# Kernel tuning notes

Hardware: AMD Instinct MI355X
Metric: run time of the kernel (lower is better)

## Reference

```python
import jax, jax.numpy as jnp
import numpy as np
from jax import lax

VOCAB = 32000
N_E = 1024
N_D = 1024
DEPTH = 4
L = 512
B = 8
HIGHWAY_BIAS = -3.0  # args.bias, folded into forget-gate bias


def setup_inputs() -> dict:
    key = jax.random.key(0)
    ks = jax.random.split(key, 8)
    x = jax.random.randint(ks[0], (L, B), 0, VOCAB)
    hidden = jnp.zeros((DEPTH, B, N_D), dtype=jnp.float32)
    emb = jax.random.normal(ks[1], (VOCAB, N_E), dtype=jnp.float32) * (3.0 / VOCAB) ** 0.5
    W0 = jax.random.normal(ks[2], (N_E, 4 * N_D), dtype=jnp.float32) * N_E ** -0.5
    Wl = jax.random.normal(ks[3], (DEPTH - 1, N_D, 3 * N_D), dtype=jnp.float32) * N_D ** -0.5
    vc = jax.random.normal(ks[4], (DEPTH, 2 * N_D), dtype=jnp.float32) * 0.1
    out_W = jax.random.normal(ks[5], (N_D, VOCAB), dtype=jnp.float32) * (3.0 / VOCAB) ** 0.5
    out_b = jnp.zeros((VOCAB,), dtype=jnp.float32)
    return {"x": x, "hidden": hidden, "emb": emb, "W0": W0, "Wl": Wl,
            "vc": vc, "out_W": out_W, "out_b": out_b}


def _sru_layer(u0, u1, u2, resid, vf, vr, c0):
    # u*: (L, B, d) precomputed GEMM outputs; scan only does elementwise recurrence.
    def step(c, inp):
        u0t, u1t, u2t, rt = inp
        f = jax.nn.sigmoid(u1t + vf * c + HIGHWAY_BIAS)
        r = jax.nn.sigmoid(u2t + vr * c)
        c_new = f * c + (1.0 - f) * u0t
        h = r * c_new + (1.0 - r) * rt
        return c_new, h
    c_last, hs = lax.scan(step, c0, (u0, u1, u2, resid))
    return hs, c_last


def reference(x, hidden, emb, W0, Wl, vc, out_W, out_b):
    h = emb[x]  # (L, B, n_e); dropout disabled (p=0)
    c_finals = []
    for layer in range(DEPTH):
        if layer == 0:
            U = jnp.einsum('lbe,ek->lbk', h, W0).reshape(L, B, 4, N_D)
            resid = U[:, :, 3]  # k=4: transformed input as highway residual
        else:
            U = jnp.einsum('lbd,dk->lbk', h, Wl[layer - 1]).reshape(L, B, 3, N_D)
            resid = h           # k=3: highway residual is the layer input
        vf = vc[layer, :N_D]
        vr = vc[layer, N_D:]
        h, c_last = _sru_layer(U[:, :, 0], U[:, :, 1], U[:, :, 2], resid, vf, vr, hidden[layer])
        c_finals.append(c_last)
    out = h.reshape(L * B, N_D) @ out_W + out_b  # (L*B, vocab)
    return out, jnp.stack(c_finals)
```

## Files before the change

kernel.cpp:

```cpp
#include <hip/hip_runtime.h>
#include <hip/hip_bf16.h>

#define L_SEQ 512
#define BATCH 8
#define ND 1024
#define VOCAB_N 32000
#define MROWS 4096
#define KDIM 1024
#define BK 64
#define NKT (KDIM / BK)
#define NKS 32
#define NSCAN 128

typedef unsigned short u16;
typedef unsigned int u32;
using bf16x8 = __attribute__((ext_vector_type(8))) __bf16;
using f32x4  = __attribute__((ext_vector_type(4))) float;
using u16x8  = __attribute__((ext_vector_type(8))) unsigned short;
using u16x4  = __attribute__((ext_vector_type(4))) unsigned short;

#define BAR() asm volatile("s_barrier" ::: "memory")
#define VMW(n) asm volatile("s_waitcnt vmcnt(" #n ")" ::: "memory")
#define SCHED() __builtin_amdgcn_sched_barrier(0)

static __device__ __forceinline__ u16 f2bf(float f) {
  u32 u = __builtin_bit_cast(u32, f);
  u32 r = u + 0x7FFF + ((u >> 16) & 1);
  return (u16)(r >> 16);
}
static __device__ __forceinline__ float bf2f(u16 b) {
  u32 u = ((u32)b) << 16;
  return __builtin_bit_cast(float, u);
}
static __device__ __forceinline__ void gload16(const void* g, void* l) {
  __builtin_amdgcn_global_load_lds(
      (const __attribute__((address_space(1))) void*)g,
      (__attribute__((address_space(3))) void*)l, 16, 0, 0);
}

static __device__ __forceinline__ void transpose_body(int tb, const float* __restrict__ W,
                                                      u16* __restrict__ Wt, int Ndim) {
  __shared__ float s[32][33];
  int nx = Ndim >> 5;
  int n0 = (tb % nx) * 32, k0 = (tb / nx) * 32;
  int tid = threadIdx.x;
  int tx = tid & 31, ty = tid >> 5;
#pragma unroll
  for (int i = 0; i < 4; i++)
    s[ty * 4 + i][tx] = __builtin_nontemporal_load(
        &W[(size_t)(k0 + ty * 4 + i) * Ndim + n0 + tx]);
  __syncthreads();
  int n = tid >> 3, kg = tid & 7;
  u16x4 o;
#pragma unroll
  for (int j = 0; j < 4; j++) o[j] = f2bf(s[kg * 4 + j][n]);
  *(u16x4*)(Wt + (size_t)(n0 + n) * KDIM + k0 + kg * 4) = o;
}

__global__ __launch_bounds__(256) void k_embed_t(const int* __restrict__ x,
                                                 const float* __restrict__ emb,
                                                 u16* __restrict__ h,
                                                 const float* __restrict__ Wsrc,
                                                 u16* __restrict__ WtOut, int NdimT) {
  if (blockIdx.x >= 2048) {
    transpose_body(blockIdx.x - 2048, Wsrc, WtOut, NdimT);
    return;
  }
  int t = blockIdx.x * 256 + threadIdx.x;
  int fidx = t * 8;
  int row = fidx >> 10;
  int col = fidx & 1023;
  int tok = x[row];
  const float4* src = (const float4*)(emb + (size_t)tok * ND + col);
  float4 a = src[0], b = src[1];
  u16x8 o;
  o[0]=f2bf(a.x); o[1]=f2bf(a.y); o[2]=f2bf(a.z); o[3]=f2bf(a.w);
  o[4]=f2bf(b.x); o[5]=f2bf(b.y); o[6]=f2bf(b.z); o[7]=f2bf(b.w);
  *(u16x8*)(h + fidx) = o;
}

__global__ __launch_bounds__(256) void k_transpose_cast(const float* __restrict__ W,
                                                        u16* __restrict__ Wt, int Ndim) {
  transpose_body(blockIdx.x, W, Wt, Ndim);
}

static __device__ __forceinline__ void stage8k(const u16* __restrict__ gbase,
                                               char* sm, int qdst, int tid) {
#pragma unroll
  for (int j = 0; j < 2; ++j) {
    int d = (j * 256 + tid) * 16;
    int o = d ^ (((d >> 7) & 7) << 4);
    gload16(gbase + (size_t)(o >> 7) * KDIM + ((o & 127) >> 1), sm + qdst + d);
  }
}

static __device__ __forceinline__ bf16x8 frag_ld(const char* sm, int base, int r, int cb) {
  int p = (r * 128 + cb) ^ ((r & 7) << 4);
  return *(const bf16x8*)(sm + base + p);
}

static __device__ __forceinline__ bf16x8 frag32(const char* smbase, int r, int cb) {
  int p = r * 64 + cb;
  p ^= ((p >> 7) & 3) << 4;
  return *(const bf16x8*)(smbase + p);
}

__global__ __launch_bounds__(512, 4) void k_gemm_out(const u16* __restrict__ A,
                                                     const u16* __restrict__ Bt,
                                                     float* __restrict__ CoutF, int Ndim,
                                                     const float* __restrict__ bias) {
  extern __shared__ __align__(16) char sm[];

  int bid = blockIdx.x;
  int xcd = bid & 7;
  int i = bid >> 3;
  int bm = (xcd << 2) | (i & 3);
  int bn = i >> 2;
  int m0 = bm * 128, n0 = bn * 256;

  int tid = threadIdx.x;
  int lane = tid & 63, w = tid >> 6;
  int wm = w >> 2, wn = w & 3;
  int l15 = lane & 15, hi16 = lane >> 4;

  f32x4 acc[4][4] = {};
  bf16x8 aA[4], bB[4];

  const u16* Ab = A + (size_t)m0 * KDIM;
  const u16* Bb = Bt + (size_t)n0 * KDIM;

  auto stage = [&](int t, int base) {
    {
      int d = tid * 16;
      int o = d ^ (((d >> 7) & 3) << 4);
      gload16(Ab + (size_t)(o >> 6) * KDIM + t * 32 + ((o & 63) >> 1), sm + base + d);
    }
#pragma unroll
    for (int j = 0; j < 2; ++j) {
      int d = (j * 512 + tid) * 16;
      int o = d ^ (((d >> 7) & 3) << 4);
      gload16(Bb + (size_t)(o >> 6) * KDIM + t * 32 + ((o & 63) >> 1),
              sm + base + 8192 + d);
    }
  };

  stage(0, 0);
  stage(1, 24576);
  VMW(3);
  BAR();

  const int cb = hi16 * 16;
  const int ra = wm * 64 + l15;
  const int rbv = wn * 64 + l15;

  int rb = 0, sb = 2;
#pragma unroll 1
  for (int t = 0; t < NKS; ++t) {
    const bool st = (t + 2 < NKS);
    if (st) stage(t + 2, sb * 24576);
    const char* cur = sm + rb * 24576;
#pragma unroll
    for (int mi = 0; mi < 4; ++mi) aA[mi] = frag32(cur, ra + mi * 16, cb);
#pragma unroll
    for (int ni = 0; ni < 4; ++ni) bB[ni] = frag32(cur + 8192, rbv + ni * 16, cb);
    __builtin_amdgcn_s_setprio(1);
#pragma unroll
    for (int mi = 0; mi < 4; ++mi)
#pragma unroll
      for (int ni = 0; ni < 4; ++ni)
        acc[mi][ni] = __builtin_amdgcn_mfma_f32_16x16x32_bf16(aA[mi], bB[ni], acc[mi][ni], 0, 0, 0);
    __builtin_amdgcn_s_setprio(0);
    SCHED();
    if (st) { VMW(3); } else { VMW(0); }
    BAR();
    rb = (rb == 2) ? 0 : rb + 1;
    sb = (sb == 2) ? 0 : sb + 1;
  }

  float* epi = (float*)sm;
  for (int p = 0; p < 4; ++p) {
    if (p) __syncthreads();
    if (wn == p) {
#pragma unroll
      for (int mi = 0; mi < 4; ++mi)
#pragma unroll
        for (int ni = 0; ni < 4; ++ni)
#pragma unroll
          for (int r = 0; r < 4; ++r)
            epi[(wm * 64 + mi * 16 + hi16 * 4 + r) * 68 + ni * 16 + l15] = acc[mi][ni][r];
    }
    __syncthreads();
    int gcolbase = n0 + p * 64;
#pragma unroll
    for (int i2 = 0; i2 < 4; ++i2) {
      int fidx = i2 * 2048 + tid * 4;
      int row = fidx >> 6, col = fidx & 63;
      f32x4 v = *(const f32x4*)(epi + row * 68 + col);
      int gcol = gcolbase + col;
      const float4 bb = *(const float4*)(bias + gcol);
      v[0] += bb.x; v[1] += bb.y; v[2] += bb.z; v[3] += bb.w;
      __builtin_nontemporal_store(v, (f32x4*)(CoutF + (size_t)(m0 + row) * Ndim + gcol));
    }
  }
}

template <int EPI>
__global__ __launch_bounds__(256, 2) void k_gemm128(const u16* __restrict__ A,
                                                    const u16* __restrict__ Bt,
                                                    u16* __restrict__ Cout, int Ndim) {
  extern __shared__ __align__(16) char sm[];

  int cpx = gridDim.x >> 3;
  int bid = blockIdx.x;
  int wg = (bid & 7) * cpx + (bid >> 3);
  int bm = wg & 31;
  int bn = wg >> 5;
  int m0 = bm * 128, n0 = bn * 128;

  int tid = threadIdx.x;
  int lane = tid & 63, w = tid >> 6;
  int wm = w >> 1, wn = w & 1;
  int l15 = lane & 15, hi16 = lane >> 4;
  const int rA = wm * 64 + l15, rB = wn * 64 + l15;

  f32x4 acc[4][4] = {};
  bf16x8 aA[4][2], bB[4][2];

  const u16* Ab = A + (size_t)m0 * KDIM;
  const u16* Bb = Bt + (size_t)n0 * KDIM;

  auto stage_tile = [&](int t, int buf) {
    int base = buf * 32768;
    stage8k(Ab + t * 64,                     sm, base,         tid);
    stage8k(Ab + (size_t)64 * KDIM + t * 64, sm, base + 8192,  tid);
    stage8k(Bb + t * 64,                     sm, base + 16384, tid);
    stage8k(Bb + (size_t)64 * KDIM + t * 64, sm, base + 24576, tid);
  };

  stage_tile(0, 0);
  VMW(0);
  BAR();

#pragma unroll 1
  for (int t = 0; t < NKT; ++t) {
    int cur = (t & 1) * 32768;
    if (t + 1 < NKT) stage_tile(t + 1, (t & 1) ^ 1);
#pragma unroll
    for (int kk = 0; kk < 2; ++kk) {
      int cb = kk * 64 + hi16 * 16;
#pragma unroll
      for (int mi = 0; mi < 4; ++mi) aA[mi][kk] = frag_ld(sm, cur, rA + mi * 16, cb);
#pragma unroll
      for (int ni = 0; ni < 4; ++ni) bB[ni][kk] = frag_ld(sm, cur + 16384, rB + ni * 16, cb);
    }
    __builtin_amdgcn_s_setprio(1);
#pragma unroll
    for (int kk = 0; kk < 2; ++kk)
#pragma unroll
      for (int mi = 0; mi < 4; ++mi)
#pragma unroll
        for (int ni = 0; ni < 4; ++ni)
          acc[mi][ni] = __builtin_amdgcn_mfma_f32_16x16x32_bf16(aA[mi][kk], bB[ni][kk], acc[mi][ni], 0, 0, 0);
    __builtin_amdgcn_s_setprio(0);
    SCHED();
    VMW(0);
    BAR();
  }

  float* epi = (float*)sm;
  for (int p = 0; p < 2; ++p) {
    if (p) __syncthreads();
    if (wn == p) {
#pragma unroll
      for (int mi = 0; mi < 4; ++mi)
#pragma unroll
        for (int ni = 0; ni < 4; ++ni)
#pragma unroll
          for (int r = 0; r < 4; ++r)
            epi[(wm * 64 + mi * 16 + hi16 * 4 + r) * 68 + ni * 16 + l15] = acc[mi][ni][r];
    }
    __syncthreads();
    int gcolbase = n0 + p * 64;
    int plane = gcolbase >> 10;
#pragma unroll
    for (int i = 0; i < 8; ++i) {
      int fidx = i * 1024 + tid * 4;
      int row = fidx >> 6, col = fidx & 63;
      f32x4 v = *(const f32x4*)(epi + row * 68 + col);
      int gcol = gcolbase + col;
      if (plane == 1) {
#pragma unroll
        for (int j = 0; j < 4; j++) v[j] = -1.44269504f * (v[j] - 3.0f);
      } else if (plane == 2) {
#pragma unroll
        for (int j = 0; j < 4; j++) v[j] = -1.44269504f * v[j];
      }
      u16x4 o;
#pragma unroll
      for (int j = 0; j < 4; j++) o[j] = f2bf(v[j]);
      *(u16x4*)(Cout + (size_t)(m0 + row) * Ndim + gcol) = o;
    }
  }
}

__global__ __launch_bounds__(256) void k_scan(const u16* __restrict__ U, int P,
                                              const u16* __restrict__ resid, int rstride,
                                              u16* __restrict__ hout,
                                              const float* __restrict__ vc,
                                              const float* __restrict__ hidden,
                                              float* __restrict__ cfin, int layer,
                                              const float* __restrict__ Wsrc,
                                              u16* __restrict__ WtOut, int NdimT) {
  if (blockIdx.x >= NSCAN) {
    transpose_body(blockIdx.x - NSCAN, Wsrc, WtOut, NdimT);
    return;
  }
  if (threadIdx.x >= 64) return;
  int cid = blockIdx.x * 64 + threadIdx.x;
  int b = cid >> 10, d = cid & 1023;
  float vfp = -1.44269504f * vc[layer * 2048 + d];
  float vrp = -1.44269504f * vc[layer * 2048 + 1024 + d];
  float c = hidden[layer * 8192 + cid];
  const u16* pu = U + (size_t)b * P * 1024 + d;
  const u16* pr = resid + (size_t)b * rstride + d;
  u16* ph = hout + (size_t)b * 1024 + d;
  const int ustep = P * 1024;
  const int rstep = rstride;

  u16 su0[16], sa1[16], sa2[16], srs[16];
#pragma unroll
  for (int j = 0; j < 16; j++) {
    su0[j] = pu[(size_t)(8 * j) * ustep];
    sa1[j] = pu[(size_t)(8 * j) * ustep + 1024];
    sa2[j] = pu[(size_t)(8 * j) * ustep + 2048];
    srs[j] = pr[(size_t)(8 * j) * rstep];
  }
  for (int tb = 0; tb < L_SEQ; tb += 16) {
#pragma unroll
    for (int j = 0; j < 16; j++) {
      int t = tb + j;
      float u0f = bf2f(su0[j]), a1f = bf2f(sa1[j]);
      float a2f = bf2f(sa2[j]), rf = bf2f(srs[j]);
      int tp = (t + 16) & 511;
      su0[j] = pu[(size_t)(8 * tp) * ustep];
      sa1[j] = pu[(size_t)(8 * tp) * ustep + 1024];
      sa2[j] = pu[(size_t)(8 * tp) * ustep + 2048];
      srs[j] = pr[(size_t)(8 * tp) * rstep];
      float e1 = __builtin_amdgcn_exp2f(fmaf(vfp, c, a1f));
      float e2 = __builtin_amdgcn_exp2f(fmaf(vrp, c, a2f));
      float fv = __builtin_amdgcn_rcpf(1.0f + e1);
      float rv = __builtin_amdgcn_rcpf(1.0f + e2);
      float cn = fmaf(fv, c - u0f, u0f);
      float hv = fmaf(rv, cn - rf, rf);
      ph[(size_t)t * (BATCH * ND)] = f2bf(hv);
      c = cn;
    }
  }
  cfin[layer * 8192 + cid] = c;
}

extern "C" void kernel_launch(void* const* d_in, const int* in_sizes, int n_in,
                              void* d_out, int out_size, void* d_ws, size_t ws_size,
                              hipStream_t stream) {
  const int*   x      = (const int*)d_in[0];
  const float* hidden = (const float*)d_in[1];
  const float* emb    = (const float*)d_in[2];
  const float* W0     = (const float*)d_in[3];
  const float* Wl     = (const float*)d_in[4];
  const float* vc     = (const float*)d_in[5];
  const float* outW   = (const float*)d_in[6];
  const float* outb   = (const float*)d_in[7];
  float* out = (float*)d_out;

  char* ws = (char*)d_ws;
  u16* hA    = (u16*)ws;
  u16* hB    = (u16*)(ws + 8388608);
  u16* U     = (u16*)(ws + 16777216);
  u16* Wt    = (u16*)(ws + 50331648);
  float* cfin = out + (size_t)MROWS * VOCAB_N;

  const size_t wtbig_off_big = 58720256;
  bool bigws = ws_size >= (size_t)(wtbig_off_big + (size_t)VOCAB_N * KDIM * 2);
  u16* WtBig = (u16*)(ws + (bigws ? wtbig_off_big : 16777216));

  k_embed_t<<<2048 + 4096, 256, 0, stream>>>(x, emb, hA, W0, Wt, 4096);

  k_gemm128<0><<<32 * 32, 256, 65536, stream>>>(hA, Wt, U, 4096);
  k_scan<<<NSCAN + 3072, 256, 0, stream>>>(U, 4, U + 3 * 1024, 4 * 1024, hB, vc, hidden,
                                           cfin, 0, Wl, Wt, 3072);

  const u16* hin[3]  = {hB, hA, hB};
  u16*       hout[3] = {hA, hB, hA};
  for (int l = 1; l <= 3; l++) {
    k_gemm128<1><<<32 * 24, 256, 65536, stream>>>(hin[l - 1], Wt, U, 3072);
    if (l < 3) {
      k_scan<<<NSCAN + 3072, 256, 0, stream>>>(U, 3, hin[l - 1], 1024, hout[l - 1], vc,
                                               hidden, cfin, l,
                                               Wl + (size_t)l * KDIM * 3072, Wt, 3072);
    } else if (bigws) {
      k_scan<<<NSCAN + 32000, 256, 0, stream>>>(U, 3, hin[l - 1], 1024, hout[l - 1], vc,
                                                hidden, cfin, l, outW, WtBig, VOCAB_N);
    } else {
      k_scan<<<NSCAN, 256, 0, stream>>>(U, 3, hin[l - 1], 1024, hout[l - 1], vc,
                                        hidden, cfin, l, nullptr, nullptr, 32);
      k_transpose_cast<<<32000, 256, 0, stream>>>(outW, WtBig, VOCAB_N);
    }
  }

  k_gemm_out<<<32 * 125, 512, 73728, stream>>>(hA, WtBig, out, VOCAB_N, outb);
}
```

Measured before the change: 665.1 us.

## Load A fragments directly from global in output GEMM, stage only B in LDS

In the output-projection GEMM kernel, the A tile is no longer staged through shared memory; each wave reads its A fragments straight from global memory into registers. The freed LDS goes to a 4-slot B buffer with prefetch depth 3 instead of 3 slots of A+B, and the B fragment loads are split into two halves to cut register pressure. The aim is to reduce LDS traffic and deepen the pipeline, at the cost of direct global loads for A that may stall MFMA issue and are duplicated across the waves that share the same rows.

Result: slower. 946.0 us (+42.2%).

```diff
diff --git a/kernel.cpp b/kernel.cpp
--- a/kernel.cpp
+++ b/kernel.cpp
@@ -124,59 +124,58 @@
   int l15 = lane & 15, hi16 = lane >> 4;
 
   f32x4 acc[4][4] = {};
-  bf16x8 aA[4], bB[4];
-
-  const u16* Ab = A + (size_t)m0 * KDIM;
+  bf16x8 aA[4], bB[2];
+
   const u16* Bb = Bt + (size_t)n0 * KDIM;
-
-  auto stage = [&](int t, int base) {
-    {
-      int d = tid * 16;
-      int o = d ^ (((d >> 7) & 3) << 4);
-      gload16(Ab + (size_t)(o >> 6) * KDIM + t * 32 + ((o & 63) >> 1), sm + base + d);
-    }
+  const u16* Ap = A + (size_t)(m0 + wm * 64 + l15) * KDIM + hi16 * 8;
+
+  auto stageB = [&](int t, int base) {
 #pragma unroll
     for (int j = 0; j < 2; ++j) {
       int d = (j * 512 + tid) * 16;
       int o = d ^ (((d >> 7) & 3) << 4);
       gload16(Bb + (size_t)(o >> 6) * KDIM + t * 32 + ((o & 63) >> 1),
-              sm + base + 8192 + d);
+              sm + base + d);
     }
   };
 
-  stage(0, 0);
-  stage(1, 24576);
-  VMW(3);
+  stageB(0, 0);
+  stageB(1, 16384);
+  stageB(2, 32768);
+  VMW(4);
   BAR();
 
   const int cb = hi16 * 16;
-  const int ra = wm * 64 + l15;
   const int rbv = wn * 64 + l15;
 
-  int rb = 0, sb = 2;
 #pragma unroll 1
   for (int t = 0; t < NKS; ++t) {
-    const bool st = (t + 2 < NKS);
-    if (st) stage(t + 2, sb * 24576);
-    const char* cur = sm + rb * 24576;
-#pragma unroll
-    for (int mi = 0; mi < 4; ++mi) aA[mi] = frag32(cur, ra + mi * 16, cb);
-#pragma unroll
-    for (int ni = 0; ni < 4; ++ni) bB[ni] = frag32(cur + 8192, rbv + ni * 16, cb);
+    const bool st = (t + 3 < NKS);
+#pragma unroll
+    for (int mi = 0; mi < 4; ++mi)
+      aA[mi] = *(const bf16x8*)(Ap + (size_t)mi * 16 * KDIM + t * 32);
+    if (st) stageB(t + 3, ((t + 3) & 3) * 16384);
+    const char* cur = sm + (t & 3) * 16384;
+
     __builtin_amdgcn_s_setprio(1);
 #pragma unroll
-    for (int mi = 0; mi < 4; ++mi)
-#pragma unroll
-      for (int ni = 0; ni < 4; ++ni)
-        acc[mi][ni] = __builtin_amdgcn_mfma_f32_16x16x32_bf16(aA[mi], bB[ni], acc[mi][ni], 0, 0, 0);
+    for (int h = 0; h < 2; ++h) {
+#pragma unroll
+      for (int j = 0; j < 2; ++j) bB[j] = frag32(cur, rbv + (h * 2 + j) * 16, cb);
+#pragma unroll
+      for (int mi = 0; mi < 4; ++mi)
+#pragma unroll
+        for (int j = 0; j < 2; ++j)
+          acc[mi][h * 2 + j] = __builtin_amdgcn_mfma_f32_16x16x32_bf16(
+              aA[mi], bB[j], acc[mi][h * 2 + j], 0, 0, 0);
+    }
     __builtin_amdgcn_s_setprio(0);
     SCHED();
-    if (st) { VMW(3); } else { VMW(0); }
+    if (st) { VMW(4); } else { VMW(0); }
     BAR();
-    rb = (rb == 2) ? 0 : rb + 1;
-    sb = (sb == 2) ? 0 : sb + 1;
-  }
-
+  }
+
+  __syncthreads();
   float* epi = (float*)sm;
   for (int p = 0; p < 4; ++p) {
     if (p) __syncthreads();
@@ -407,5 +406,5 @@
     }
   }
 
-  k_gemm_out<<<32 * 125, 512, 73728, stream>>>(hA, WtBig, out, VOCAB_N, outb);
-}
+  k_gemm_out<<<32 * 125, 512, 65536, stream>>>(hA, WtBig, out, VOCAB_N, outb);
+}
```

## Switch layer GEMM to triple-buffered BK=32 pipeline with XCD-aware tile mapping

Applied to the files above, without the earlier changes.

The 128x128 layer GEMM now stages K-tiles of 32 instead of 64 and keeps three shared-memory buffers, prefetching two tiles ahead and waiting only on the older loads (vmcnt 4) rather than draining all loads every iteration. Shared memory per block falls from 64KB to 48KB, and the launch bound rises to 3 blocks per CU so occupancy can increase. The block-to-tile mapping is changed so each XCD handles a contiguous group of M tiles, which should improve L2 reuse of the A operand. In exchange there are twice as many barriers per K-loop, and fewer registers are available per thread.

Result: no change. 657.2 us (-1.2%).

```diff
diff --git a/kernel.cpp b/kernel.cpp
--- a/kernel.cpp
+++ b/kernel.cpp
@@ -7,8 +7,6 @@
 #define VOCAB_N 32000
 #define MROWS 4096
 #define KDIM 1024
-#define BK 64
-#define NKT (KDIM / BK)
 #define NKS 32
 #define NSCAN 128
 
@@ -84,21 +82,6 @@
   transpose_body(blockIdx.x, W, Wt, Ndim);
 }
 
-static __device__ __forceinline__ void stage8k(const u16* __restrict__ gbase,
-                                               char* sm, int qdst, int tid) {
-#pragma unroll
-  for (int j = 0; j < 2; ++j) {
-    int d = (j * 256 + tid) * 16;
-    int o = d ^ (((d >> 7) & 7) << 4);
-    gload16(gbase + (size_t)(o >> 7) * KDIM + ((o & 127) >> 1), sm + qdst + d);
-  }
-}
-
-static __device__ __forceinline__ bf16x8 frag_ld(const char* sm, int base, int r, int cb) {
-  int p = (r * 128 + cb) ^ ((r & 7) << 4);
-  return *(const bf16x8*)(sm + base + p);
-}
-
 static __device__ __forceinline__ bf16x8 frag32(const char* smbase, int r, int cb) {
   int p = r * 64 + cb;
   p ^= ((p >> 7) & 3) << 4;
@@ -205,66 +188,76 @@
 }
 
 template <int EPI>
-__global__ __launch_bounds__(256, 2) void k_gemm128(const u16* __restrict__ A,
+__global__ __launch_bounds__(256, 3) void k_gemm128(const u16* __restrict__ A,
                                                     const u16* __restrict__ Bt,
                                                     u16* __restrict__ Cout, int Ndim) {
   extern __shared__ __align__(16) char sm[];
 
-  int cpx = gridDim.x >> 3;
   int bid = blockIdx.x;
-  int wg = (bid & 7) * cpx + (bid >> 3);
-  int bm = wg & 31;
-  int bn = wg >> 5;
+  int xcd = bid & 7;
+  int i = bid >> 3;
+  int bm = (xcd << 2) | (i & 3);
+  int bn = i >> 2;
   int m0 = bm * 128, n0 = bn * 128;
 
   int tid = threadIdx.x;
   int lane = tid & 63, w = tid >> 6;
   int wm = w >> 1, wn = w & 1;
   int l15 = lane & 15, hi16 = lane >> 4;
-  const int rA = wm * 64 + l15, rB = wn * 64 + l15;
 
   f32x4 acc[4][4] = {};
-  bf16x8 aA[4][2], bB[4][2];
+  bf16x8 aA[4], bB[4];
 
   const u16* Ab = A + (size_t)m0 * KDIM;
   const u16* Bb = Bt + (size_t)n0 * KDIM;
 
-  auto stage_tile = [&](int t, int buf) {
-    int base = buf * 32768;
-    stage8k(Ab + t * 64,                     sm, base,         tid);
-    stage8k(Ab + (size_t)64 * KDIM + t * 64, sm, base + 8192,  tid);
-    stage8k(Bb + t * 64,                     sm, base + 16384, tid);
-    stage8k(Bb + (size_t)64 * KDIM + t * 64, sm, base + 24576, tid);
+  auto stage = [&](int t, int base) {
+#pragma unroll
+    for (int j = 0; j < 2; ++j) {
+      int d = (j * 256 + tid) * 16;
+      int o = d ^ (((d >> 7) & 3) << 4);
+      gload16(Ab + (size_t)(o >> 6) * KDIM + t * 32 + ((o & 63) >> 1), sm + base + d);
+    }
+#pragma unroll
+    for (int j = 0; j < 2; ++j) {
+      int d = (j * 256 + tid) * 16;
+      int o = d ^ (((d >> 7) & 3) << 4);
+      gload16(Bb + (size_t)(o >> 6) * KDIM + t * 32 + ((o & 63) >> 1),
+              sm + base + 8192 + d);
+    }
   };
 
-  stage_tile(0, 0);
-  VMW(0);
+  stage(0, 0);
+  stage(1, 16384);
+  VMW(4);
   BAR();
 
+  const int cb = hi16 * 16;
+  const int ra = wm * 64 + l15;
+  const int rbv = wn * 64 + l15;
+
+  int rb = 0, sb = 2;
 #pragma unroll 1
-  for (int t = 0; t < NKT; ++t) {
-    int cur = (t & 1) * 32768;
-    if (t + 1 < NKT) stage_tile(t + 1, (t & 1) ^ 1);
-#pragma unroll
-    for (int kk = 0; kk < 2; ++kk) {
-      int cb = kk * 64 + hi16 * 16;
-#pragma unroll
-      for (int mi = 0; mi < 4; ++mi) aA[mi][kk] = frag_ld(sm, cur, rA + mi * 16, cb);
-#pragma unroll
-      for (int ni = 0; ni < 4; ++ni) bB[ni][kk] = frag_ld(sm, cur + 16384, rB + ni * 16, cb);
-    }
+  for (int t = 0; t < NKS; ++t) {
+    const bool st = (t + 2 < NKS);
+    if (st) stage(t + 2, sb * 16384);
+    const char* cur = sm + rb * 16384;
+#pragma unroll
+    for (int mi = 0; mi < 4; ++mi) aA[mi] = frag32(cur, ra + mi * 16, cb);
+#pragma unroll
+    for (int ni = 0; ni < 4; ++ni) bB[ni] = frag32(cur + 8192, rbv + ni * 16, cb);
     __builtin_amdgcn_s_setprio(1);
 #pragma unroll
-    for (int kk = 0; kk < 2; ++kk)
-#pragma unroll
-      for (int mi = 0; mi < 4; ++mi)
-#pragma unroll
-        for (int ni = 0; ni < 4; ++ni)
-          acc[mi][ni] = __builtin_amdgcn_mfma_f32_16x16x32_bf16(aA[mi][kk], bB[ni][kk], acc[mi][ni], 0, 0, 0);
+    for (int mi = 0; mi < 4; ++mi)
+#pragma unroll
+      for (int ni = 0; ni < 4; ++ni)
+        acc[mi][ni] = __builtin_amdgcn_mfma_f32_16x16x32_bf16(aA[mi], bB[ni], acc[mi][ni], 0, 0, 0);
     __builtin_amdgcn_s_setprio(0);
     SCHED();
-    VMW(0);
+    if (st) { VMW(4); } else { VMW(0); }
     BAR();
+    rb = (rb == 2) ? 0 : rb + 1;
+    sb = (sb == 2) ? 0 : sb + 1;
   }
 
   float* epi = (float*)sm;
@@ -283,8 +276,8 @@
     int gcolbase = n0 + p * 64;
     int plane = gcolbase >> 10;
 #pragma unroll
-    for (int i = 0; i < 8; ++i) {
-      int fidx = i * 1024 + tid * 4;
+    for (int i2 = 0; i2 < 8; ++i2) {
+      int fidx = i2 * 1024 + tid * 4;
       int row = fidx >> 6, col = fidx & 63;
       f32x4 v = *(const f32x4*)(epi + row * 68 + col);
       int gcol = gcolbase + col;
@@ -385,14 +378,14 @@
 
   k_embed_t<<<2048 + 4096, 256, 0, stream>>>(x, emb, hA, W0, Wt, 4096);
 
-  k_gemm128<0><<<32 * 32, 256, 65536, stream>>>(hA, Wt, U, 4096);
+  k_gemm128<0><<<32 * 32, 256, 49152, stream>>>(hA, Wt, U, 4096);
   k_scan<<<NSCAN + 3072, 256, 0, stream>>>(U, 4, U + 3 * 1024, 4 * 1024, hB, vc, hidden,
                                            cfin, 0, Wl, Wt, 3072);
 
   const u16* hin[3]  = {hB, hA, hB};
   u16*       hout[3] = {hA, hB, hA};
   for (int l = 1; l <= 3; l++) {
-    k_gemm128<1><<<32 * 24, 256, 65536, stream>>>(hin[l - 1], Wt, U, 3072);
+    k_gemm128<1><<<32 * 24, 256, 49152, stream>>>(hin[l - 1], Wt, U, 3072);
     if (l < 3) {
       k_scan<<<NSCAN + 3072, 256, 0, stream>>>(U, 3, hin[l - 1], 1024, hout[l - 1], vc,
                                                hidden, cfin, l,
```
